# Kernel optimization log

Hardware: AMD Instinct MI355X
Metric: run time of the kernel (lower is better)

Reference implementation:

```python
import jax, jax.numpy as jnp
import numpy as np

TAU = 0.07
EPS = 1e-6  # torch CosineSimilarity eps


def setup_inputs() -> dict:
    key = jax.random.key(0)
    k1, k2, k3 = jax.random.split(key, 3)
    n, d, n_classes = 8192, 256, 1024
    imitation_embeds = jax.random.normal(k1, (n, d), dtype=jnp.float32)
    recording_embeds = jax.random.normal(k2, (n, d), dtype=jnp.float32)
    labels = jax.random.randint(k3, (n,), 0, n_classes, dtype=jnp.int64)
    return {
        "imitation_embeds": imitation_embeds,
        "recording_embeds": recording_embeds,
        "labels": labels,
    }


def reference(imitation_embeds, recording_embeds, labels):
    n = imitation_embeds.shape[0]
    # cosine similarity with per-vector norm clamp (torch semantics)
    im_n = imitation_embeds / jnp.maximum(
        jnp.linalg.norm(imitation_embeds, axis=1, keepdims=True), EPS)
    rec_n = recording_embeds / jnp.maximum(
        jnp.linalg.norm(recording_embeds, axis=1, keepdims=True), EPS)
    i2r = jnp.einsum("nd,md->nm", im_n, rec_n) / TAU  # [n, n]

    same = labels[:, None] == labels[None, :]          # [n, n] bool
    eye = jnp.eye(n, dtype=bool)
    # original: mask = ~(same ^ diag_embed(diag(same))); diag(same) is all True
    # -> keep the diagonal (positive) and all different-label negatives
    mask = ~(same ^ eye)

    # per-row masked log-softmax evaluated at the diagonal entry:
    # log_softmax(row[mask])[pos_of_diag] = i2r[i,i] - logsumexp(row over mask)
    lse = jax.nn.logsumexp(jnp.where(mask, i2r, -jnp.inf), axis=1)  # [n]
    loss = -jnp.mean(jnp.diagonal(i2r) - lse)
    return loss
```

## Files before the change

kernel.cpp:

```cpp
#include <hip/hip_runtime.h>

#define N 8192
#define D 256
#define INV_TAU 14.285714285714286f
#define SCALE2 20.60992915555662f
#define EPSN 1e-6f
#define MAXM 48

#define RT 256
#define CT 64
#define CSPLIT 16
#define CPB (N / CSPLIT)
#define NTILES (CPB / CT)

typedef unsigned int u32x4 __attribute__((ext_vector_type(4)));
typedef __bf16 bf16x8 __attribute__((ext_vector_type(8)));
typedef float f32x4 __attribute__((ext_vector_type(4)));

__device__ inline unsigned short f2bf(float x) {
    unsigned int u = __builtin_bit_cast(unsigned int, x);
    u += 0x7fffu + ((u >> 16) & 1u);
    return (unsigned short)(u >> 16);
}
__device__ inline float b2f(unsigned short u) {
    unsigned int x = (unsigned int)u << 16;
    return __builtin_bit_cast(float, x);
}
__device__ inline float fexp2(float x) {
#if __has_builtin(__builtin_amdgcn_exp2f)
    return __builtin_amdgcn_exp2f(x);
#else
    return __expf(x * 0.6931471805599453f);
#endif
}

__global__ void ntx_prep(const float* __restrict__ im, const float* __restrict__ rec,
                         const int* __restrict__ labels,
                         unsigned short* __restrict__ A, unsigned short* __restrict__ Bm,
                         float* __restrict__ diag, float* __restrict__ rowsum,
                         int* __restrict__ cnt, unsigned short* __restrict__ members) {
    const int wave = threadIdx.x >> 6;
    const int lane = threadIdx.x & 63;
    const int row  = blockIdx.x * 4 + wave;

    const float4 a = ((const float4*)(im  + (size_t)row * D))[lane];
    const float4 b = ((const float4*)(rec + (size_t)row * D))[lane];

    float ssa = a.x*a.x + a.y*a.y + a.z*a.z + a.w*a.w;
    float ssb = b.x*b.x + b.y*b.y + b.z*b.z + b.w*b.w;
    float dt  = a.x*b.x + a.y*b.y + a.z*b.z + a.w*b.w;
    #pragma unroll
    for (int o = 32; o; o >>= 1) {
        ssa += __shfl_xor(ssa, o);
        ssb += __shfl_xor(ssb, o);
        dt  += __shfl_xor(dt , o);
    }
    const float ra = 1.0f / fmaxf(sqrtf(ssa), EPSN);
    const float rb = 1.0f / fmaxf(sqrtf(ssb), EPSN);

    ushort4 pa, pb;
    pa.x = f2bf(a.x*ra); pa.y = f2bf(a.y*ra); pa.z = f2bf(a.z*ra); pa.w = f2bf(a.w*ra);
    pb.x = f2bf(b.x*rb); pb.y = f2bf(b.y*rb); pb.z = f2bf(b.z*rb); pb.w = f2bf(b.w*rb);

    *(ushort4*)(A + (size_t)row * D + lane * 4) = pa;
    const int chunk = lane >> 1;
    const int sw = chunk ^ (row & 7);
    *(ushort4*)(Bm + (size_t)row * D + sw * 8 + (lane & 1) * 4) = pb;

    if (lane == 0) {
        diag[row]   = dt * ra * rb * INV_TAU;
        rowsum[row] = 0.0f;
        const int lab = labels[row];
        const int u = atomicAdd(&cnt[lab], 1);
        if (u < MAXM) members[lab * MAXM + u] = (unsigned short)row;
    }
}

__global__ __launch_bounds__(256, 2)
void ntx_lse(const unsigned short* __restrict__ A, const unsigned short* __restrict__ Bm,
             float* __restrict__ rowsum) {
    __shared__ __align__(16) unsigned short Bs[CT][D];

    const int wave = threadIdx.x >> 6;
    const int lane = threadIdx.x & 63;
    const int g    = lane >> 4;
    const int n16  = lane & 15;

    const int rowblk = blockIdx.x & (N / RT - 1);
    const int colblk = blockIdx.x >> 5;
    const int row0 = rowblk * RT + wave * 64;
    const int col0 = colblk * CPB;

    bf16x8 afrag[4][8];
    #pragma unroll
    for (int rs = 0; rs < 4; ++rs) {
        const int r = row0 + rs * 16 + n16;
        #pragma unroll
        for (int k = 0; k < 8; ++k)
            afrag[rs][k] = __builtin_bit_cast(
                bf16x8, *(const u32x4*)(A + (size_t)r * D + k * 32 + g * 8));
    }

    float acc[4][4];
    #pragma unroll
    for (int rs = 0; rs < 4; ++rs)
        #pragma unroll
        for (int q = 0; q < 4; ++q) acc[rs][q] = 0.f;

    for (int t = 0; t < NTILES; ++t) {
        const char* gsrc = (const char*)(Bm + (size_t)(col0 + t * CT) * D);
        char* lbase = (char*)&Bs[0][0];
        #pragma unroll
        for (int i = 0; i < 8; ++i) {
            const int off = (i * 4 + wave) * 1024;
            __builtin_amdgcn_global_load_lds(
                (const __attribute__((address_space(1))) void*)(gsrc + off + lane * 16),
                (__attribute__((address_space(3))) void*)(lbase + off),
                16, 0, 0);
        }
        __syncthreads();

        #pragma unroll
        for (int cs = 0; cs < 4; ++cs) {
            const int bc = cs * 16 + n16;
            bf16x8 bfrag[8];
            #pragma unroll
            for (int k = 0; k < 8; ++k)
                bfrag[k] = __builtin_bit_cast(
                    bf16x8, *(const u32x4*)(&Bs[bc][((k * 4 + g) ^ (bc & 7)) * 8]));

            #pragma unroll
            for (int rs = 0; rs < 4; ++rs) {
                f32x4 c = {0.f, 0.f, 0.f, 0.f};
                #pragma unroll
                for (int k = 0; k < 8; ++k)
                    c = __builtin_amdgcn_mfma_f32_16x16x32_bf16(
                            afrag[rs][k], bfrag[k], c, 0, 0, 0);
                #pragma unroll
                for (int q = 0; q < 4; ++q)
                    acc[rs][q] += fexp2(c[q] * SCALE2);
            }
        }
        __syncthreads();
    }

    #pragma unroll
    for (int rs = 0; rs < 4; ++rs)
        #pragma unroll
        for (int q = 0; q < 4; ++q) {
            float v = acc[rs][q];
            v += __shfl_xor(v, 1);
            v += __shfl_xor(v, 2);
            v += __shfl_xor(v, 4);
            v += __shfl_xor(v, 8);
            if (n16 == 0)
                atomicAdd(&rowsum[row0 + rs * 16 + g * 4 + q], v);
        }
}

__global__ void ntx_correct(const unsigned short* __restrict__ A,
                            const unsigned short* __restrict__ Bm,
                            const int* __restrict__ labels, const int* __restrict__ cnt,
                            const unsigned short* __restrict__ members,
                            float* __restrict__ rowsum) {
    const int wave = threadIdx.x >> 6;
    const int lane = threadIdx.x & 63;
    const int W = blockIdx.x * 4 + wave;
    const int chunk = lane >> 1;

    for (int rr = 0; rr < 4; ++rr) {
        const int r = W * 4 + rr;
        const int lab = labels[r];
        const int m = min(cnt[lab], MAXM);
        const ushort4 av = *(const ushort4*)(A + (size_t)r * D + lane * 4);
        const float a0 = b2f(av.x), a1 = b2f(av.y), a2 = b2f(av.z), a3 = b2f(av.w);
        float sum = 0.f;
        for (int t = 0; t < m; ++t) {
            const int j = members[lab * MAXM + t];
            if (j == r) continue;
            const int sw = chunk ^ (j & 7);
            const ushort4 bv = *(const ushort4*)(Bm + (size_t)j * D + sw * 8 + (lane & 1) * 4);
            float d = a0 * b2f(bv.x) + a1 * b2f(bv.y) + a2 * b2f(bv.z) + a3 * b2f(bv.w);
            #pragma unroll
            for (int o = 32; o; o >>= 1) d += __shfl_xor(d, o);
            sum += fexp2(d * SCALE2);
        }
        if (lane == 0) rowsum[r] -= sum;
    }
}

__global__ void ntx_finish(const float* __restrict__ diag,
                           const float* __restrict__ rowsum,
                           float* __restrict__ out) {
    __shared__ float red[256];
    float s = 0.f;
    for (int i = threadIdx.x; i < N; i += 256)
        s += logf(rowsum[i]) - diag[i];
    red[threadIdx.x] = s;
    __syncthreads();
    #pragma unroll
    for (int o = 128; o; o >>= 1) {
        if (threadIdx.x < o) red[threadIdx.x] += red[threadIdx.x + o];
        __syncthreads();
    }
    if (threadIdx.x == 0) out[0] = red[0] / (float)N;
}

extern "C" void kernel_launch(void* const* d_in, const int* in_sizes, int n_in,
                              void* d_out, int out_size, void* d_ws, size_t ws_size,
                              hipStream_t stream) {
    const float* im     = (const float*)d_in[0];
    const float* rec    = (const float*)d_in[1];
    const int*   labels = (const int*)d_in[2];
    float* out = (float*)d_out;

    unsigned short* A  = (unsigned short*)d_ws;
    unsigned short* Bm = A + (size_t)N * D;
    float* diag   = (float*)(Bm + (size_t)N * D);
    float* rowsum = diag + N;
    int* cnt      = (int*)(rowsum + N);
    unsigned short* members = (unsigned short*)(cnt + 1024);

    hipMemsetAsync(cnt, 0, 1024 * sizeof(int), stream);
    ntx_prep<<<N / 4, 256, 0, stream>>>(im, rec, labels, A, Bm, diag, rowsum, cnt, members);
    ntx_lse<<<(N / RT) * CSPLIT, 256, 0, stream>>>(A, Bm, rowsum);
    ntx_correct<<<N / 16, 256, 0, stream>>>(A, Bm, labels, cnt, members, rowsum);
    ntx_finish<<<1, 256, 0, stream>>>(diag, rowsum, out);
}
```

Before: 149.7 us.

## Double-buffer LDS tiles, fold scale into A, fuse correction and finish per class

The LSE kernel now double-buffers the B tile in LDS, issuing the next tile's loads before computing on the current one, and drops one barrier per iteration. The log2-domain scale is folded into the normalised A rows in prep, which removes a multiply per exp. The label grouping pass (memset plus atomics in prep) is replaced by a per-class block that scans the labels, computes the same-label correction pairs, and reduces the log-sum term directly, so the separate single-block finish kernel goes away. The costs are a 1024-block label scan that reads all N labels per block, extra LDS for the second buffer, bf16 rounding of the pre-scaled A values, and a final atomic accumulation.

New measurement: 151.0 us. About the same (+0.8%).

```diff
diff --git a/kernel.cpp b/kernel.cpp
--- a/kernel.cpp
+++ b/kernel.cpp
@@ -4,8 +4,9 @@
 #define D 256
 #define INV_TAU 14.285714285714286f
 #define SCALE2 20.60992915555662f
+#define LN2F 0.6931471805599453f
 #define EPSN 1e-6f
-#define MAXM 48
+#define MAXM 128
 
 #define RT 256
 #define CT 64
@@ -35,10 +36,9 @@
 }
 
 __global__ void ntx_prep(const float* __restrict__ im, const float* __restrict__ rec,
-                         const int* __restrict__ labels,
                          unsigned short* __restrict__ A, unsigned short* __restrict__ Bm,
                          float* __restrict__ diag, float* __restrict__ rowsum,
-                         int* __restrict__ cnt, unsigned short* __restrict__ members) {
+                         float* __restrict__ acc) {
     const int wave = threadIdx.x >> 6;
     const int lane = threadIdx.x & 63;
     const int row  = blockIdx.x * 4 + wave;
@@ -55,8 +55,8 @@
         ssb += __shfl_xor(ssb, o);
         dt  += __shfl_xor(dt , o);
     }
-    const float ra = 1.0f / fmaxf(sqrtf(ssa), EPSN);
-    const float rb = 1.0f / fmaxf(sqrtf(ssb), EPSN);
+    const float ra = SCALE2 / fmaxf(sqrtf(ssa), EPSN);
+    const float rb = 1.0f   / fmaxf(sqrtf(ssb), EPSN);
 
     ushort4 pa, pb;
     pa.x = f2bf(a.x*ra); pa.y = f2bf(a.y*ra); pa.z = f2bf(a.z*ra); pa.w = f2bf(a.w*ra);
@@ -68,18 +68,16 @@
     *(ushort4*)(Bm + (size_t)row * D + sw * 8 + (lane & 1) * 4) = pb;
 
     if (lane == 0) {
-        diag[row]   = dt * ra * rb * INV_TAU;
+        diag[row]   = (dt / SCALE2) * ra * rb * INV_TAU;
         rowsum[row] = 0.0f;
-        const int lab = labels[row];
-        const int u = atomicAdd(&cnt[lab], 1);
-        if (u < MAXM) members[lab * MAXM + u] = (unsigned short)row;
+        if (row == 0) acc[0] = 0.0f;
     }
 }
 
 __global__ __launch_bounds__(256, 2)
 void ntx_lse(const unsigned short* __restrict__ A, const unsigned short* __restrict__ Bm,
              float* __restrict__ rowsum) {
-    __shared__ __align__(16) unsigned short Bs[CT][D];
+    __shared__ __align__(16) unsigned short Bs[2][CT][D];
 
     const int wave = threadIdx.x >> 6;
     const int lane = threadIdx.x & 63;
@@ -107,18 +105,28 @@
         #pragma unroll
         for (int q = 0; q < 4; ++q) acc[rs][q] = 0.f;
 
+    const char* gbase = (const char*)(Bm + (size_t)col0 * D);
+
+    #define STAGE(t, buf)                                                          \
+        {                                                                          \
+            const char* gsrc = gbase + (t) * (CT * D * 2);                         \
+            char* lbase = (char*)&Bs[buf][0][0];                                   \
+            _Pragma("unroll")                                                      \
+            for (int i = 0; i < 8; ++i) {                                          \
+                const int off = (i * 4 + wave) * 1024;                             \
+                __builtin_amdgcn_global_load_lds(                                  \
+                    (const __attribute__((address_space(1))) void*)(gsrc + off + lane * 16), \
+                    (__attribute__((address_space(3))) void*)(lbase + off),        \
+                    16, 0, 0);                                                     \
+            }                                                                      \
+        }
+
+    STAGE(0, 0)
+
     for (int t = 0; t < NTILES; ++t) {
-        const char* gsrc = (const char*)(Bm + (size_t)(col0 + t * CT) * D);
-        char* lbase = (char*)&Bs[0][0];
-        #pragma unroll
-        for (int i = 0; i < 8; ++i) {
-            const int off = (i * 4 + wave) * 1024;
-            __builtin_amdgcn_global_load_lds(
-                (const __attribute__((address_space(1))) void*)(gsrc + off + lane * 16),
-                (__attribute__((address_space(3))) void*)(lbase + off),
-                16, 0, 0);
-        }
         __syncthreads();
+        if (t + 1 < NTILES) STAGE(t + 1, (t + 1) & 1)
+        const int buf = t & 1;
 
         #pragma unroll
         for (int cs = 0; cs < 4; ++cs) {
@@ -127,7 +135,7 @@
             #pragma unroll
             for (int k = 0; k < 8; ++k)
                 bfrag[k] = __builtin_bit_cast(
-                    bf16x8, *(const u32x4*)(&Bs[bc][((k * 4 + g) ^ (bc & 7)) * 8]));
+                    bf16x8, *(const u32x4*)(&Bs[buf][bc][((k * 4 + g) ^ (bc & 7)) * 8]));
 
             #pragma unroll
             for (int rs = 0; rs < 4; ++rs) {
@@ -138,10 +146,9 @@
                             afrag[rs][k], bfrag[k], c, 0, 0, 0);
                 #pragma unroll
                 for (int q = 0; q < 4; ++q)
-                    acc[rs][q] += fexp2(c[q] * SCALE2);
+                    acc[rs][q] += fexp2(c[q]);
             }
         }
-        __syncthreads();
     }
 
     #pragma unroll
@@ -158,52 +165,66 @@
         }
 }
 
-__global__ void ntx_correct(const unsigned short* __restrict__ A,
-                            const unsigned short* __restrict__ Bm,
-                            const int* __restrict__ labels, const int* __restrict__ cnt,
-                            const unsigned short* __restrict__ members,
-                            float* __restrict__ rowsum) {
+__global__ void ntx_ccf(const unsigned short* __restrict__ A,
+                        const unsigned short* __restrict__ Bm,
+                        const int* __restrict__ labels,
+                        const float* __restrict__ diag,
+                        const float* __restrict__ rowsum,
+                        float* __restrict__ acc) {
+    __shared__ int   rows[MAXM];
+    __shared__ float corr[MAXM];
+    __shared__ int   mcnt;
+    __shared__ float wred[4];
+
+    const int c = blockIdx.x;
+    if (threadIdx.x == 0) mcnt = 0;
+    __syncthreads();
+
+    for (int i = threadIdx.x; i < N; i += 256)
+        if (labels[i] == c) {
+            const int u = atomicAdd(&mcnt, 1);
+            if (u < MAXM) rows[u] = i;
+        }
+    __syncthreads();
+    const int m = min(mcnt, MAXM);
+    for (int i = threadIdx.x; i < m; i += 256) corr[i] = 0.f;
+    __syncthreads();
+
     const int wave = threadIdx.x >> 6;
     const int lane = threadIdx.x & 63;
-    const int W = blockIdx.x * 4 + wave;
     const int chunk = lane >> 1;
 
-    for (int rr = 0; rr < 4; ++rr) {
-        const int r = W * 4 + rr;
-        const int lab = labels[r];
-        const int m = min(cnt[lab], MAXM);
+    for (int p = wave; p < m * m; p += 4) {
+        const int i = p / m, j = p - i * m;
+        if (i == j) continue;
+        const int r  = rows[i];
+        const int jr = rows[j];
         const ushort4 av = *(const ushort4*)(A + (size_t)r * D + lane * 4);
-        const float a0 = b2f(av.x), a1 = b2f(av.y), a2 = b2f(av.z), a3 = b2f(av.w);
-        float sum = 0.f;
-        for (int t = 0; t < m; ++t) {
-            const int j = members[lab * MAXM + t];
-            if (j == r) continue;
-            const int sw = chunk ^ (j & 7);
-            const ushort4 bv = *(const ushort4*)(Bm + (size_t)j * D + sw * 8 + (lane & 1) * 4);
-            float d = a0 * b2f(bv.x) + a1 * b2f(bv.y) + a2 * b2f(bv.z) + a3 * b2f(bv.w);
-            #pragma unroll
-            for (int o = 32; o; o >>= 1) d += __shfl_xor(d, o);
-            sum += fexp2(d * SCALE2);
-        }
-        if (lane == 0) rowsum[r] -= sum;
-    }
-}
-
-__global__ void ntx_finish(const float* __restrict__ diag,
-                           const float* __restrict__ rowsum,
-                           float* __restrict__ out) {
-    __shared__ float red[256];
-    float s = 0.f;
-    for (int i = threadIdx.x; i < N; i += 256)
-        s += logf(rowsum[i]) - diag[i];
-    red[threadIdx.x] = s;
-    __syncthreads();
-    #pragma unroll
-    for (int o = 128; o; o >>= 1) {
-        if (threadIdx.x < o) red[threadIdx.x] += red[threadIdx.x + o];
-        __syncthreads();
-    }
-    if (threadIdx.x == 0) out[0] = red[0] / (float)N;
+        const int sw = chunk ^ (jr & 7);
+        const ushort4 bv = *(const ushort4*)(Bm + (size_t)jr * D + sw * 8 + (lane & 1) * 4);
+        float d = b2f(av.x)*b2f(bv.x) + b2f(av.y)*b2f(bv.y)
+                + b2f(av.z)*b2f(bv.z) + b2f(av.w)*b2f(bv.w);
+        #pragma unroll
+        for (int o = 32; o; o >>= 1) d += __shfl_xor(d, o);
+        if (lane == 0) atomicAdd(&corr[i], fexp2(d));
+    }
+    __syncthreads();
+
+    float v = 0.f;
+    for (int i = threadIdx.x; i < m; i += 256) {
+        const int r = rows[i];
+        v += log2f(rowsum[r] - corr[i]) * LN2F - diag[r];
+    }
+    #pragma unroll
+    for (int o = 32; o; o >>= 1) v += __shfl_xor(v, o);
+    if (lane == 0) wred[wave] = v;
+    __syncthreads();
+    if (threadIdx.x == 0)
+        atomicAdd(acc, wred[0] + wred[1] + wred[2] + wred[3]);
+}
+
+__global__ void ntx_final(const float* __restrict__ acc, float* __restrict__ out) {
+    out[0] = acc[0] / (float)N;
 }
 
 extern "C" void kernel_launch(void* const* d_in, const int* in_sizes, int n_in,
@@ -218,12 +239,10 @@
     unsigned short* Bm = A + (size_t)N * D;
     float* diag   = (float*)(Bm + (size_t)N * D);
     float* rowsum = diag + N;
-    int* cnt      = (int*)(rowsum + N);
-    unsigned short* members = (unsigned short*)(cnt + 1024);
-
-    hipMemsetAsync(cnt, 0, 1024 * sizeof(int), stream);
-    ntx_prep<<<N / 4, 256, 0, stream>>>(im, rec, labels, A, Bm, diag, rowsum, cnt, members);
+    float* acc    = rowsum + N;
+
+    ntx_prep<<<N / 4, 256, 0, stream>>>(im, rec, A, Bm, diag, rowsum, acc);
     ntx_lse<<<(N / RT) * CSPLIT, 256, 0, stream>>>(A, Bm, rowsum);
-    ntx_correct<<<N / 16, 256, 0, stream>>>(A, Bm, labels, cnt, members, rowsum);
-    ntx_finish<<<1, 256, 0, stream>>>(diag, rowsum, out);
-}
+    ntx_ccf<<<1024, 256, 0, stream>>>(A, Bm, labels, diag, rowsum, acc);
+    ntx_final<<<1, 1, 0, stream>>>(acc, out);
+}
```
